# Optimization experiments

Measured on AMD Instinct MI355X. Metric: run time of the kernel, lower is better.

Reference implementation:

```python
import jax, jax.numpy as jnp
import numpy as np

B, T, D = 2, 2048, 1024
N, H = 16, 64  # num_heads, head_dim


def setup_inputs() -> dict:
    key = jax.random.key(0)
    ks = jax.random.split(key, 8)
    glorot = lambda k, shape, fan_in, fan_out: jax.random.uniform(
        k, shape, jnp.float32, -1.0, 1.0) * np.sqrt(6.0 / (fan_in + fan_out))
    return {
        "q": jax.random.normal(ks[0], (B, T, D), jnp.float32),
        "v": jax.random.normal(ks[1], (B, T, D), jnp.float32),
        "k": jax.random.normal(ks[2], (B, T, D), jnp.float32),
        "w_query": glorot(ks[3], (D, N, H), D, N * H),
        "b_query": jnp.zeros((N, 1, H), jnp.float32),
        "w_value": glorot(ks[4], (D, N, H), D, N * H),
        "b_value": jnp.zeros((N, 1, H), jnp.float32),
        "w_key": glorot(ks[5], (D, N, H), D, N * H),
        "b_key": jnp.zeros((N, 1, H), jnp.float32),
        "w_projection": glorot(ks[6], (N, D, H), N * H, D),
        "b_projection": jnp.zeros((1, D), jnp.float32),
    }


def reference(q, v, k, w_query, b_query, w_value, b_value, w_key, b_key,
              w_projection, b_projection):
    # QKV projections: [B,T,D] x [D,N,H] -> [B,N,T,H]
    query = jnp.einsum('btd,dnh->bnth', q, w_query) + b_query
    value = jnp.einsum('btd,dnh->bnth', v, w_value) + b_value
    key_p = jnp.einsum('btd,dnh->bnth', k, w_key) + b_key
    # Scaled dot-product attention, scores divided by sqrt(head_dim)
    scale = 1.0 / jnp.sqrt(jnp.asarray(H, query.dtype))
    scores = jnp.einsum('bnth,bnsh->bnts', query, key_p) * scale  # [B,N,T,T]
    weights = jax.nn.softmax(scores, axis=-1)
    attn = jnp.einsum('bnts,bnsh->bnth', weights, value)
    # Output projection: [B,N,T,H] x [N,D,H] -> [B,T,D]
    out = jnp.einsum('bnth,ndh->btd', attn, w_projection) + b_projection
    return out
```

## Files before the change

### kernel.cpp

```cpp
#include <hip/hip_runtime.h>
#include <hip/hip_bf16.h>
#include <cstdint>
#include <cstddef>


typedef __attribute__((ext_vector_type(8))) short short8;
typedef __attribute__((ext_vector_type(4))) float floatx4;
typedef __attribute__((ext_vector_type(8))) unsigned short ushort8;

#define EXP2F(x) __builtin_amdgcn_exp2f(x)

static __device__ __forceinline__ unsigned short f2bf(float f) {
    union { float f; unsigned int u; } v; v.f = f;
    unsigned int r = v.u + 0x7fffu + ((v.u >> 16) & 1u);
    return (unsigned short)(r >> 16);
}
static __device__ __forceinline__ unsigned int pk2bf(float lo, float hi) {
    __hip_bfloat162 t = __float22bfloat162_rn(make_float2(lo, hi));
    union { __hip_bfloat162 h; unsigned int u; } c; c.h = t;
    return c.u;
}
static __device__ __forceinline__ void gl_lds16(const unsigned short* g, unsigned short* l) {
    __builtin_amdgcn_global_load_lds(
        (const __attribute__((address_space(1))) unsigned int*)g,
        (__attribute__((address_space(3))) unsigned int*)l, 16, 0, 0);
}

__global__ __launch_bounds__(256) void mha_transpose_w(
    const float* __restrict__ wq, const float* __restrict__ wk, const float* __restrict__ wv,
    unsigned short* __restrict__ wqT, unsigned short* __restrict__ wkT, unsigned short* __restrict__ wvT)
{
    __shared__ float tile[32][33];
    const float* src; unsigned short* dst;
    int z = blockIdx.z;
    if (z == 0)      { src = wq; dst = wqT; }
    else if (z == 1) { src = wk; dst = wkT; }
    else             { src = wv; dst = wvT; }
    int n0 = blockIdx.x * 32, d0 = blockIdx.y * 32;
    int tx = threadIdx.x, ty = threadIdx.y;
    #pragma unroll
    for (int j = 0; j < 4; ++j)
        tile[ty + j * 8][tx] = src[(size_t)(d0 + ty + j * 8) * 1024 + n0 + tx];
    __syncthreads();
    #pragma unroll
    for (int j = 0; j < 4; ++j)
        dst[(size_t)(n0 + ty + j * 8) * 1024 + d0 + tx] = f2bf(tile[tx][ty + j * 8]);
}

__global__ __launch_bounds__(256) void mha_reorder_wp(
    const float* __restrict__ wp, unsigned short* __restrict__ wp2)
{
    int base = blockIdx.x * 1024 + threadIdx.x;
    #pragma unroll
    for (int i = 0; i < 4; ++i) {
        int idx = base + i * 256;
        int n = idx >> 16, d = (idx >> 6) & 1023, h = idx & 63;
        wp2[(size_t)d * 1024 + n * 64 + h] = f2bf(wp[idx]);
    }
}

__global__ __launch_bounds__(256) void prep_bf16(
    const float* __restrict__ x, unsigned short* __restrict__ xb)
{
    size_t i = ((size_t)blockIdx.x * 256 + threadIdx.x) * 8;
    float4 a = *(const float4*)(x + i);
    float4 b = *(const float4*)(x + i + 4);
    uint4 o;
    o.x = pk2bf(a.x, a.y); o.y = pk2bf(a.z, a.w);
    o.z = pk2bf(b.x, b.y); o.w = pk2bf(b.z, b.w);
    *(uint4*)(xb + i) = o;
}

__global__ __launch_bounds__(256) void gemm_qkv64(
    const unsigned short* __restrict__ A0, const unsigned short* __restrict__ A1,
    const unsigned short* __restrict__ A2,
    const unsigned short* __restrict__ W0, const unsigned short* __restrict__ W1,
    const unsigned short* __restrict__ W2,
    const float* __restrict__ b0, const float* __restrict__ b1, const float* __restrict__ b2,
    unsigned short* __restrict__ O0, unsigned short* __restrict__ O1, unsigned short* __restrict__ O2,
    float qscale, int matSel)
{
    __shared__ unsigned short As[64 * 32];
    __shared__ unsigned short Bs[128 * 32];
    int bm = blockIdx.x, by = blockIdx.y;
    int mat, nt;
    if (matSel < 0) { mat = by >> 3; nt = by & 7; } else { mat = matSel; nt = by; }
    const unsigned short* A  = mat == 0 ? A0 : (mat == 1 ? A1 : A2);
    const unsigned short* WT = mat == 0 ? W0 : (mat == 1 ? W1 : W2);
    const float* bias        = mat == 0 ? b0 : (mat == 1 ? b1 : b2);
    unsigned short* Out      = mat == 0 ? O0 : (mat == 1 ? O1 : O2);
    float scale = (mat == 0) ? qscale : 1.0f;
    int vmode = (mat == 2);

    int tid = threadIdx.x;
    int w = tid >> 6, lane = tid & 63, c15 = lane & 15, quad = lane >> 4;
    int wm = w >> 1, wn = w & 1;

    const unsigned short* gsrc[3];
    unsigned short* ldst[3];
    #pragma unroll
    for (int j = 0; j < 3; ++j) {
        int c = w * 3 + j;
        if (c < 4) {
            gsrc[j] = A + (size_t)(bm * 64 + c * 16 + (lane >> 2)) * 1024 + (lane & 3) * 8;
            ldst[j] = &As[c * 512 + lane * 8];
        } else {
            int d = c - 4;
            gsrc[j] = WT + (size_t)(nt * 128 + d * 16 + (lane >> 2)) * 1024 + (lane & 3) * 8;
            ldst[j] = &Bs[d * 512 + lane * 8];
        }
    }

    floatx4 acc[2][4];
    #pragma unroll
    for (int mi = 0; mi < 2; ++mi)
        #pragma unroll
        for (int ni = 0; ni < 4; ++ni) acc[mi][ni] = (floatx4){0.f, 0.f, 0.f, 0.f};

    for (int kt = 0; kt < 32; ++kt) {
        __syncthreads();
        #pragma unroll
        for (int j = 0; j < 3; ++j) gl_lds16(gsrc[j] + kt * 32, ldst[j]);
        __syncthreads();
        short8 af[2], bfr[4];
        #pragma unroll
        for (int mi = 0; mi < 2; ++mi)
            af[mi] = *(const short8*)&As[(wm * 32 + mi * 16 + c15) * 32 + quad * 8];
        #pragma unroll
        for (int ni = 0; ni < 4; ++ni)
            bfr[ni] = *(const short8*)&Bs[(wn * 64 + ni * 16 + c15) * 32 + quad * 8];
        #pragma unroll
        for (int mi = 0; mi < 2; ++mi)
            #pragma unroll
            for (int ni = 0; ni < 4; ++ni)
                acc[mi][ni] = __builtin_amdgcn_mfma_f32_16x16x32_bf16(af[mi], bfr[ni], acc[mi][ni], 0, 0, 0);
    }
    #pragma unroll
    for (int mi = 0; mi < 2; ++mi)
        #pragma unroll
        for (int ni = 0; ni < 4; ++ni)
            #pragma unroll
            for (int r = 0; r < 4; ++r) {
                int row = bm * 64 + wm * 32 + mi * 16 + quad * 4 + r;
                int col = nt * 128 + wn * 64 + ni * 16 + c15;
                float val = (acc[mi][ni][r] + bias[col]) * scale;
                int b = row >> 11, t = row & 2047, n = col >> 6, h = col & 63;
                if (vmode)
                    Out[((size_t)(b * 16 + n) * 64 + h) * 2048 + t] = f2bf(val);
                else
                    Out[((size_t)(b * 16 + n) * 2048 + t) * 64 + h] = f2bf(val);
            }
}

__global__ __launch_bounds__(256) void mha_flash3(
    const unsigned short* __restrict__ Qp, const unsigned short* __restrict__ Kp,
    const unsigned short* __restrict__ Vt, unsigned short* __restrict__ attnb)
{
    __shared__ unsigned short Ks[64 * 72];
    __shared__ unsigned short Vs[64 * 72];
    __shared__ unsigned short Pl[4][32 * 72];

    int bi = blockIdx.x;
    int bn = bi >> 4, qt = bi & 15;
    int b = bn >> 4, n = bn & 15;
    int tid = threadIdx.x;
    int w = tid >> 6, lane = tid & 63, c15 = lane & 15, quad = lane >> 4;

    const unsigned short* Qb = Qp + (size_t)bn * 2048 * 64;
    const unsigned short* Kb = Kp + (size_t)bn * 2048 * 64;
    const unsigned short* Vb = Vt + (size_t)bn * 64 * 2048;

    int qbase = qt * 128 + w * 32;

    short8 bQ[2][2];
    #pragma unroll
    for (int tni = 0; tni < 2; ++tni)
        #pragma unroll
        for (int kc = 0; kc < 2; ++kc)
            bQ[tni][kc] = *(const short8*)(Qb + (size_t)(qbase + tni * 16 + c15) * 64 + kc * 32 + quad * 8);

    float l_i[2] = {0.f, 0.f};
    floatx4 o[2][4];
    #pragma unroll
    for (int i = 0; i < 2; ++i)
        #pragma unroll
        for (int j = 0; j < 4; ++j) o[i][j] = (floatx4){0.f, 0.f, 0.f, 0.f};

    unsigned short* Pw = &Pl[w][0];
    int srow = tid >> 3, scc = tid & 7;

    ushort8 kreg[2], vreg[2];
    #pragma unroll
    for (int i = 0; i < 2; ++i) {
        kreg[i] = *(const ushort8*)(Kb + (size_t)(srow + i * 32) * 64 + scc * 8);
        vreg[i] = *(const ushort8*)(Vb + (size_t)(srow + i * 32) * 2048 + scc * 8);
    }

    for (int it = 0; it < 32; ++it) {
        __syncthreads();
        #pragma unroll
        for (int i = 0; i < 2; ++i) {
            *(ushort8*)&Ks[(srow + i * 32) * 72 + scc * 8] = kreg[i];
            *(ushort8*)&Vs[(srow + i * 32) * 72 + scc * 8] = vreg[i];
        }
        if (it < 31) {
            int s1 = (it + 1) * 64;
            #pragma unroll
            for (int i = 0; i < 2; ++i) {
                kreg[i] = *(const ushort8*)(Kb + (size_t)(s1 + srow + i * 32) * 64 + scc * 8);
                vreg[i] = *(const ushort8*)(Vb + (size_t)(srow + i * 32) * 2048 + s1 + scc * 8);
            }
        }
        __syncthreads();

        floatx4 sc[4][2];
        #pragma unroll
        for (int smi = 0; smi < 4; ++smi) {
            short8 a0 = *(const short8*)&Ks[(smi * 16 + c15) * 72 + quad * 8];
            short8 a1 = *(const short8*)&Ks[(smi * 16 + c15) * 72 + 32 + quad * 8];
            #pragma unroll
            for (int tni = 0; tni < 2; ++tni) {
                floatx4 t = (floatx4){0.f, 0.f, 0.f, 0.f};
                t = __builtin_amdgcn_mfma_f32_16x16x32_bf16(a0, bQ[tni][0], t, 0, 0, 0);
                t = __builtin_amdgcn_mfma_f32_16x16x32_bf16(a1, bQ[tni][1], t, 0, 0, 0);
                sc[smi][tni] = t;
            }
        }
        #pragma unroll
        for (int tni = 0; tni < 2; ++tni) {
            float rs = 0.f;
            #pragma unroll
            for (int smi = 0; smi < 4; ++smi) {
                float p0 = EXP2F(sc[smi][tni][0]);
                float p1 = EXP2F(sc[smi][tni][1]);
                float p2 = EXP2F(sc[smi][tni][2]);
                float p3 = EXP2F(sc[smi][tni][3]);
                rs += (p0 + p1) + (p2 + p3);
                uint2 pw;
                pw.x = pk2bf(p0, p1);
                pw.y = pk2bf(p2, p3);
                *(uint2*)&Pw[(tni * 16 + c15) * 72 + smi * 16 + quad * 4] = pw;
            }
            l_i[tni] += rs;
        }
        short8 bv[4][2];
        #pragma unroll
        for (int hni = 0; hni < 4; ++hni)
            #pragma unroll
            for (int kc = 0; kc < 2; ++kc)
                bv[hni][kc] = *(const short8*)&Vs[(hni * 16 + c15) * 72 + kc * 32 + quad * 8];
        #pragma unroll
        for (int tmi = 0; tmi < 2; ++tmi) {
            short8 ap0 = *(const short8*)&Pw[(tmi * 16 + c15) * 72 + quad * 8];
            short8 ap1 = *(const short8*)&Pw[(tmi * 16 + c15) * 72 + 32 + quad * 8];
            #pragma unroll
            for (int hni = 0; hni < 4; ++hni) {
                o[tmi][hni] = __builtin_amdgcn_mfma_f32_16x16x32_bf16(ap0, bv[hni][0], o[tmi][hni], 0, 0, 0);
                o[tmi][hni] = __builtin_amdgcn_mfma_f32_16x16x32_bf16(ap1, bv[hni][1], o[tmi][hni], 0, 0, 0);
            }
        }
    }
    float lf[2];
    #pragma unroll
    for (int tmi = 0; tmi < 2; ++tmi) {
        float s = l_i[tmi];
        s += __shfl_xor(s, 16, 64);
        s += __shfl_xor(s, 32, 64);
        lf[tmi] = s;
    }
    #pragma unroll
    for (int tmi = 0; tmi < 2; ++tmi)
        #pragma unroll
        for (int r = 0; r < 4; ++r) {
            float linv = 1.0f / __shfl(lf[tmi], quad * 4 + r, 64);
            int t = qbase + tmi * 16 + quad * 4 + r;
            #pragma unroll
            for (int hni = 0; hni < 4; ++hni) {
                int col = n * 64 + hni * 16 + c15;
                attnb[(size_t)(b * 2048 + t) * 1024 + col] = f2bf(o[tmi][hni][r] * linv);
            }
        }
}

__global__ __launch_bounds__(256) void gemm_out64(
    const unsigned short* __restrict__ A, const unsigned short* __restrict__ BT,
    const float* __restrict__ bias, float* __restrict__ out)
{
    __shared__ unsigned short As[64 * 32];
    __shared__ unsigned short Bs[128 * 32];
    int bm = blockIdx.x, nt = blockIdx.y;
    int tid = threadIdx.x;
    int w = tid >> 6, lane = tid & 63, c15 = lane & 15, quad = lane >> 4;
    int wm = w >> 1, wn = w & 1;

    const unsigned short* gsrc[3];
    unsigned short* ldst[3];
    #pragma unroll
    for (int j = 0; j < 3; ++j) {
        int c = w * 3 + j;
        if (c < 4) {
            gsrc[j] = A + (size_t)(bm * 64 + c * 16 + (lane >> 2)) * 1024 + (lane & 3) * 8;
            ldst[j] = &As[c * 512 + lane * 8];
        } else {
            int d = c - 4;
            gsrc[j] = BT + (size_t)(nt * 128 + d * 16 + (lane >> 2)) * 1024 + (lane & 3) * 8;
            ldst[j] = &Bs[d * 512 + lane * 8];
        }
    }

    floatx4 acc[2][4];
    #pragma unroll
    for (int mi = 0; mi < 2; ++mi)
        #pragma unroll
        for (int ni = 0; ni < 4; ++ni) acc[mi][ni] = (floatx4){0.f, 0.f, 0.f, 0.f};

    for (int kt = 0; kt < 32; ++kt) {
        __syncthreads();
        #pragma unroll
        for (int j = 0; j < 3; ++j) gl_lds16(gsrc[j] + kt * 32, ldst[j]);
        __syncthreads();
        short8 af[2], bfr[4];
        #pragma unroll
        for (int mi = 0; mi < 2; ++mi)
            af[mi] = *(const short8*)&As[(wm * 32 + mi * 16 + c15) * 32 + quad * 8];
        #pragma unroll
        for (int ni = 0; ni < 4; ++ni)
            bfr[ni] = *(const short8*)&Bs[(wn * 64 + ni * 16 + c15) * 32 + quad * 8];
        #pragma unroll
        for (int mi = 0; mi < 2; ++mi)
            #pragma unroll
            for (int ni = 0; ni < 4; ++ni)
                acc[mi][ni] = __builtin_amdgcn_mfma_f32_16x16x32_bf16(af[mi], bfr[ni], acc[mi][ni], 0, 0, 0);
    }
    #pragma unroll
    for (int mi = 0; mi < 2; ++mi)
        #pragma unroll
        for (int ni = 0; ni < 4; ++ni)
            #pragma unroll
            for (int r = 0; r < 4; ++r) {
                int row = bm * 64 + wm * 32 + mi * 16 + quad * 4 + r;
                int col = nt * 128 + wn * 64 + ni * 16 + c15;
                out[(size_t)row * 1024 + col] = acc[mi][ni][r] + bias[col];
            }
}

extern "C" void kernel_launch(void* const* d_in, const int* in_sizes, int n_in,
                              void* d_out, int out_size, void* d_ws, size_t ws_size,
                              hipStream_t stream)
{
    const float* q  = (const float*)d_in[0];
    const float* v  = (const float*)d_in[1];
    const float* k  = (const float*)d_in[2];
    const float* wq = (const float*)d_in[3];
    const float* bq = (const float*)d_in[4];
    const float* wv = (const float*)d_in[5];
    const float* bv = (const float*)d_in[6];
    const float* wk = (const float*)d_in[7];
    const float* bk = (const float*)d_in[8];
    const float* wp = (const float*)d_in[9];
    const float* bp = (const float*)d_in[10];
    float* out = (float*)d_out;

    char* ws = (char*)d_ws;
    unsigned short* wqT  = (unsigned short*)(ws + (size_t)0);
    unsigned short* wkT  = (unsigned short*)(ws + ((size_t)2  << 20));
    unsigned short* wvT  = (unsigned short*)(ws + ((size_t)4  << 20));
    unsigned short* wp2  = (unsigned short*)(ws + ((size_t)6  << 20));
    unsigned short* Qp   = (unsigned short*)(ws + ((size_t)8  << 20));
    unsigned short* Kp   = (unsigned short*)(ws + ((size_t)16 << 20));
    unsigned short* Vtp  = (unsigned short*)(ws + ((size_t)24 << 20));
    unsigned short* Xb   = (unsigned short*)(ws + ((size_t)32 << 20));
    unsigned short* attnb= (unsigned short*)(ws + ((size_t)32 << 20));

    const float qscale = 0.125f * 1.44269504088896f;

    hipLaunchKernelGGL(mha_transpose_w, dim3(32, 32, 3), dim3(32, 8), 0, stream,
                       wq, wk, wv, wqT, wkT, wvT);
    hipLaunchKernelGGL(mha_reorder_wp, dim3(1024), dim3(256), 0, stream, wp, wp2);

    if (ws_size >= ((size_t)64 << 20)) {
        unsigned short* qb = (unsigned short*)(ws + ((size_t)40 << 20));
        unsigned short* kb = (unsigned short*)(ws + ((size_t)48 << 20));
        unsigned short* vb = (unsigned short*)(ws + ((size_t)56 << 20));
        hipLaunchKernelGGL(prep_bf16, dim3(2048), dim3(256), 0, stream, q, qb);
        hipLaunchKernelGGL(prep_bf16, dim3(2048), dim3(256), 0, stream, k, kb);
        hipLaunchKernelGGL(prep_bf16, dim3(2048), dim3(256), 0, stream, v, vb);
        hipLaunchKernelGGL(gemm_qkv64, dim3(64, 24), dim3(256), 0, stream,
                           qb, kb, vb, wqT, wkT, wvT, bq, bk, bv, Qp, Kp, Vtp, qscale, -1);
    } else {
        hipLaunchKernelGGL(prep_bf16, dim3(2048), dim3(256), 0, stream, q, Xb);
        hipLaunchKernelGGL(gemm_qkv64, dim3(64, 8), dim3(256), 0, stream,
                           Xb, Xb, Xb, wqT, wkT, wvT, bq, bk, bv, Qp, Kp, Vtp, qscale, 0);
        hipLaunchKernelGGL(prep_bf16, dim3(2048), dim3(256), 0, stream, k, Xb);
        hipLaunchKernelGGL(gemm_qkv64, dim3(64, 8), dim3(256), 0, stream,
                           Xb, Xb, Xb, wqT, wkT, wvT, bq, bk, bv, Qp, Kp, Vtp, qscale, 1);
        hipLaunchKernelGGL(prep_bf16, dim3(2048), dim3(256), 0, stream, v, Xb);
        hipLaunchKernelGGL(gemm_qkv64, dim3(64, 8), dim3(256), 0, stream,
                           Xb, Xb, Xb, wqT, wkT, wvT, bq, bk, bv, Qp, Kp, Vtp, qscale, 2);
    }

    hipLaunchKernelGGL(mha_flash3, dim3(512), dim3(256), 0, stream, Qp, Kp, Vtp, attnb);
    hipLaunchKernelGGL(gemm_out64, dim3(64, 8), dim3(256), 0, stream, attnb, wp2, bp, out);
}
```

Measured before the change: 251.7 us.

## Enlarge QKV GEMM tile, swizzle out-GEMM LDS, fuse prep launches, remap flash blocks to XCDs

The three bf16 conversion launches are merged into one 2D-grid kernel. The QKV GEMM moves to a 128x128 tile (4x4 MFMA per wave) for more data reuse per block, and the output GEMM takes a K-step of 64 with an XOR-swizzled LDS layout to reduce bank conflicts. The flash attention block index is remapped so that blocks sharing a head land on the same XCD, which should improve L2 locality. Larger tiles raise register and LDS pressure and halve the QKV grid, which may hurt occupancy.

```diff
diff --git a/kernel.cpp b/kernel.cpp
--- a/kernel.cpp
+++ b/kernel.cpp
@@ -59,19 +59,23 @@
     }
 }
 
-__global__ __launch_bounds__(256) void prep_bf16(
-    const float* __restrict__ x, unsigned short* __restrict__ xb)
-{
+__global__ __launch_bounds__(256) void prep_bf16_3(
+    const float* __restrict__ x0, const float* __restrict__ x1, const float* __restrict__ x2,
+    unsigned short* __restrict__ o0, unsigned short* __restrict__ o1, unsigned short* __restrict__ o2)
+{
+    int y = blockIdx.y;
+    const float* x = y == 0 ? x0 : (y == 1 ? x1 : x2);
+    unsigned short* o = y == 0 ? o0 : (y == 1 ? o1 : o2);
     size_t i = ((size_t)blockIdx.x * 256 + threadIdx.x) * 8;
     float4 a = *(const float4*)(x + i);
     float4 b = *(const float4*)(x + i + 4);
-    uint4 o;
-    o.x = pk2bf(a.x, a.y); o.y = pk2bf(a.z, a.w);
-    o.z = pk2bf(b.x, b.y); o.w = pk2bf(b.z, b.w);
-    *(uint4*)(xb + i) = o;
-}
-
-__global__ __launch_bounds__(256) void gemm_qkv64(
+    uint4 pk;
+    pk.x = pk2bf(a.x, a.y); pk.y = pk2bf(a.z, a.w);
+    pk.z = pk2bf(b.x, b.y); pk.w = pk2bf(b.z, b.w);
+    *(uint4*)(o + i) = pk;
+}
+
+__global__ __launch_bounds__(256) void gemm_qkv128(
     const unsigned short* __restrict__ A0, const unsigned short* __restrict__ A1,
     const unsigned short* __restrict__ A2,
     const unsigned short* __restrict__ W0, const unsigned short* __restrict__ W1,
@@ -80,7 +84,7 @@
     unsigned short* __restrict__ O0, unsigned short* __restrict__ O1, unsigned short* __restrict__ O2,
     float qscale, int matSel)
 {
-    __shared__ unsigned short As[64 * 32];
+    __shared__ unsigned short As[128 * 32];
     __shared__ unsigned short Bs[128 * 32];
     int bm = blockIdx.x, by = blockIdx.y;
     int mat, nt;
@@ -96,52 +100,48 @@
     int w = tid >> 6, lane = tid & 63, c15 = lane & 15, quad = lane >> 4;
     int wm = w >> 1, wn = w & 1;
 
-    const unsigned short* gsrc[3];
-    unsigned short* ldst[3];
-    #pragma unroll
-    for (int j = 0; j < 3; ++j) {
-        int c = w * 3 + j;
-        if (c < 4) {
-            gsrc[j] = A + (size_t)(bm * 64 + c * 16 + (lane >> 2)) * 1024 + (lane & 3) * 8;
-            ldst[j] = &As[c * 512 + lane * 8];
-        } else {
-            int d = c - 4;
-            gsrc[j] = WT + (size_t)(nt * 128 + d * 16 + (lane >> 2)) * 1024 + (lane & 3) * 8;
-            ldst[j] = &Bs[d * 512 + lane * 8];
-        }
-    }
-
-    floatx4 acc[2][4];
-    #pragma unroll
-    for (int mi = 0; mi < 2; ++mi)
+    const unsigned short* gA[2]; unsigned short* lA[2];
+    const unsigned short* gB[2]; unsigned short* lB[2];
+    #pragma unroll
+    for (int i = 0; i < 2; ++i) {
+        int s = (w * 2 + i) * 64 + lane;
+        gA[i] = A  + (size_t)(bm * 128 + (s >> 2)) * 1024 + (s & 3) * 8;
+        lA[i] = &As[s * 8];
+        gB[i] = WT + (size_t)(nt * 128 + (s >> 2)) * 1024 + (s & 3) * 8;
+        lB[i] = &Bs[s * 8];
+    }
+
+    floatx4 acc[4][4];
+    #pragma unroll
+    for (int mi = 0; mi < 4; ++mi)
         #pragma unroll
         for (int ni = 0; ni < 4; ++ni) acc[mi][ni] = (floatx4){0.f, 0.f, 0.f, 0.f};
 
     for (int kt = 0; kt < 32; ++kt) {
         __syncthreads();
         #pragma unroll
-        for (int j = 0; j < 3; ++j) gl_lds16(gsrc[j] + kt * 32, ldst[j]);
-        __syncthreads();
-        short8 af[2], bfr[4];
-        #pragma unroll
-        for (int mi = 0; mi < 2; ++mi)
-            af[mi] = *(const short8*)&As[(wm * 32 + mi * 16 + c15) * 32 + quad * 8];
+        for (int i = 0; i < 2; ++i) { gl_lds16(gA[i] + kt * 32, lA[i]); gl_lds16(gB[i] + kt * 32, lB[i]); }
+        __syncthreads();
+        short8 af[4], bfr[4];
+        #pragma unroll
+        for (int mi = 0; mi < 4; ++mi)
+            af[mi] = *(const short8*)&As[(wm * 64 + mi * 16 + c15) * 32 + quad * 8];
         #pragma unroll
         for (int ni = 0; ni < 4; ++ni)
             bfr[ni] = *(const short8*)&Bs[(wn * 64 + ni * 16 + c15) * 32 + quad * 8];
         #pragma unroll
-        for (int mi = 0; mi < 2; ++mi)
+        for (int mi = 0; mi < 4; ++mi)
             #pragma unroll
             for (int ni = 0; ni < 4; ++ni)
                 acc[mi][ni] = __builtin_amdgcn_mfma_f32_16x16x32_bf16(af[mi], bfr[ni], acc[mi][ni], 0, 0, 0);
     }
     #pragma unroll
-    for (int mi = 0; mi < 2; ++mi)
+    for (int mi = 0; mi < 4; ++mi)
         #pragma unroll
         for (int ni = 0; ni < 4; ++ni)
             #pragma unroll
             for (int r = 0; r < 4; ++r) {
-                int row = bm * 64 + wm * 32 + mi * 16 + quad * 4 + r;
+                int row = bm * 128 + wm * 64 + mi * 16 + quad * 4 + r;
                 int col = nt * 128 + wn * 64 + ni * 16 + c15;
                 float val = (acc[mi][ni][r] + bias[col]) * scale;
                 int b = row >> 11, t = row & 2047, n = col >> 6, h = col & 63;
@@ -161,7 +161,8 @@
     __shared__ unsigned short Pl[4][32 * 72];
 
     int bi = blockIdx.x;
-    int bn = bi >> 4, qt = bi & 15;
+    int xcd = bi & 7, j = bi >> 3;
+    int bn = xcd * 4 + (j >> 4), qt = j & 15;
     int b = bn >> 4, n = bn & 15;
     int tid = threadIdx.x;
     int w = tid >> 6, lane = tid & 63, c15 = lane & 15, quad = lane >> 4;
@@ -184,7 +185,7 @@
     #pragma unroll
     for (int i = 0; i < 2; ++i)
         #pragma unroll
-        for (int j = 0; j < 4; ++j) o[i][j] = (floatx4){0.f, 0.f, 0.f, 0.f};
+        for (int j2 = 0; j2 < 4; ++j2) o[i][j2] = (floatx4){0.f, 0.f, 0.f, 0.f};
 
     unsigned short* Pw = &Pl[w][0];
     int srow = tid >> 3, scc = tid & 7;
@@ -282,30 +283,32 @@
         }
 }
 
-__global__ __launch_bounds__(256) void gemm_out64(
+__global__ __launch_bounds__(256) void gemm_out64v2(
     const unsigned short* __restrict__ A, const unsigned short* __restrict__ BT,
     const float* __restrict__ bias, float* __restrict__ out)
 {
-    __shared__ unsigned short As[64 * 32];
-    __shared__ unsigned short Bs[128 * 32];
+    __shared__ unsigned short As[64 * 64];
+    __shared__ unsigned short Bs[128 * 64];
     int bm = blockIdx.x, nt = blockIdx.y;
     int tid = threadIdx.x;
     int w = tid >> 6, lane = tid & 63, c15 = lane & 15, quad = lane >> 4;
     int wm = w >> 1, wn = w & 1;
 
-    const unsigned short* gsrc[3];
-    unsigned short* ldst[3];
-    #pragma unroll
-    for (int j = 0; j < 3; ++j) {
-        int c = w * 3 + j;
-        if (c < 4) {
-            gsrc[j] = A + (size_t)(bm * 64 + c * 16 + (lane >> 2)) * 1024 + (lane & 3) * 8;
-            ldst[j] = &As[c * 512 + lane * 8];
-        } else {
-            int d = c - 4;
-            gsrc[j] = BT + (size_t)(nt * 128 + d * 16 + (lane >> 2)) * 1024 + (lane & 3) * 8;
-            ldst[j] = &Bs[d * 512 + lane * 8];
-        }
+    const unsigned short* gA[2]; unsigned short* lA[2];
+    const unsigned short* gB[4]; unsigned short* lB[4];
+    #pragma unroll
+    for (int i = 0; i < 2; ++i) {
+        int s = (w * 2 + i) * 64 + lane;
+        int row = s >> 3, cl = (s & 7) ^ (row & 7);
+        gA[i] = A + (size_t)(bm * 64 + row) * 1024 + cl * 8;
+        lA[i] = &As[s * 8];
+    }
+    #pragma unroll
+    for (int i = 0; i < 4; ++i) {
+        int s = (w * 4 + i) * 64 + lane;
+        int row = s >> 3, cl = (s & 7) ^ (row & 7);
+        gB[i] = BT + (size_t)(nt * 128 + row) * 1024 + cl * 8;
+        lB[i] = &Bs[s * 8];
     }
 
     floatx4 acc[2][4];
@@ -314,23 +317,32 @@
         #pragma unroll
         for (int ni = 0; ni < 4; ++ni) acc[mi][ni] = (floatx4){0.f, 0.f, 0.f, 0.f};
 
-    for (int kt = 0; kt < 32; ++kt) {
-        __syncthreads();
-        #pragma unroll
-        for (int j = 0; j < 3; ++j) gl_lds16(gsrc[j] + kt * 32, ldst[j]);
-        __syncthreads();
-        short8 af[2], bfr[4];
-        #pragma unroll
-        for (int mi = 0; mi < 2; ++mi)
-            af[mi] = *(const short8*)&As[(wm * 32 + mi * 16 + c15) * 32 + quad * 8];
-        #pragma unroll
-        for (int ni = 0; ni < 4; ++ni)
-            bfr[ni] = *(const short8*)&Bs[(wn * 64 + ni * 16 + c15) * 32 + quad * 8];
-        #pragma unroll
-        for (int mi = 0; mi < 2; ++mi)
-            #pragma unroll
-            for (int ni = 0; ni < 4; ++ni)
-                acc[mi][ni] = __builtin_amdgcn_mfma_f32_16x16x32_bf16(af[mi], bfr[ni], acc[mi][ni], 0, 0, 0);
+    for (int kt = 0; kt < 16; ++kt) {
+        __syncthreads();
+        #pragma unroll
+        for (int i = 0; i < 2; ++i) gl_lds16(gA[i] + kt * 64, lA[i]);
+        #pragma unroll
+        for (int i = 0; i < 4; ++i) gl_lds16(gB[i] + kt * 64, lB[i]);
+        __syncthreads();
+        #pragma unroll
+        for (int kc = 0; kc < 2; ++kc) {
+            short8 af[2], bfr[4];
+            #pragma unroll
+            for (int mi = 0; mi < 2; ++mi) {
+                int row = wm * 32 + mi * 16 + c15;
+                af[mi] = *(const short8*)&As[row * 64 + (((kc * 4 + quad) ^ (row & 7)) * 8)];
+            }
+            #pragma unroll
+            for (int ni = 0; ni < 4; ++ni) {
+                int row = wn * 64 + ni * 16 + c15;
+                bfr[ni] = *(const short8*)&Bs[row * 64 + (((kc * 4 + quad) ^ (row & 7)) * 8)];
+            }
+            #pragma unroll
+            for (int mi = 0; mi < 2; ++mi)
+                #pragma unroll
+                for (int ni = 0; ni < 4; ++ni)
+                    acc[mi][ni] = __builtin_amdgcn_mfma_f32_16x16x32_bf16(af[mi], bfr[ni], acc[mi][ni], 0, 0, 0);
+        }
     }
     #pragma unroll
     for (int mi = 0; mi < 2; ++mi)
@@ -382,23 +394,21 @@
         unsigned short* qb = (unsigned short*)(ws + ((size_t)40 << 20));
         unsigned short* kb = (unsigned short*)(ws + ((size_t)48 << 20));
         unsigned short* vb = (unsigned short*)(ws + ((size_t)56 << 20));
-        hipLaunchKernelGGL(prep_bf16, dim3(2048), dim3(256), 0, stream, q, qb);
-        hipLaunchKernelGGL(prep_bf16, dim3(2048), dim3(256), 0, stream, k, kb);
-        hipLaunchKernelGGL(prep_bf16, dim3(2048), dim3(256), 0, stream, v, vb);
-        hipLaunchKernelGGL(gemm_qkv64, dim3(64, 24), dim3(256), 0, stream,
+        hipLaunchKernelGGL(prep_bf16_3, dim3(2048, 3), dim3(256), 0, stream, q, k, v, qb, kb, vb);
+        hipLaunchKernelGGL(gemm_qkv128, dim3(32, 24), dim3(256), 0, stream,
                            qb, kb, vb, wqT, wkT, wvT, bq, bk, bv, Qp, Kp, Vtp, qscale, -1);
     } else {
-        hipLaunchKernelGGL(prep_bf16, dim3(2048), dim3(256), 0, stream, q, Xb);
-        hipLaunchKernelGGL(gemm_qkv64, dim3(64, 8), dim3(256), 0, stream,
+        hipLaunchKernelGGL(prep_bf16_3, dim3(2048, 1), dim3(256), 0, stream, q, q, q, Xb, Xb, Xb);
+        hipLaunchKernelGGL(gemm_qkv128, dim3(32, 8), dim3(256), 0, stream,
                            Xb, Xb, Xb, wqT, wkT, wvT, bq, bk, bv, Qp, Kp, Vtp, qscale, 0);
-        hipLaunchKernelGGL(prep_bf16, dim3(2048), dim3(256), 0, stream, k, Xb);
-        hipLaunchKernelGGL(gemm_qkv64, dim3(64, 8), dim3(256), 0, stream,
+        hipLaunchKernelGGL(prep_bf16_3, dim3(2048, 1), dim3(256), 0, stream, k, k, k, Xb, Xb, Xb);
+        hipLaunchKernelGGL(gemm_qkv128, dim3(32, 8), dim3(256), 0, stream,
                            Xb, Xb, Xb, wqT, wkT, wvT, bq, bk, bv, Qp, Kp, Vtp, qscale, 1);
-        hipLaunchKernelGGL(prep_bf16, dim3(2048), dim3(256), 0, stream, v, Xb);
-        hipLaunchKernelGGL(gemm_qkv64, dim3(64, 8), dim3(256), 0, stream,
+        hipLaunchKernelGGL(prep_bf16_3, dim3(2048, 1), dim3(256), 0, stream, v, v, v, Xb, Xb, Xb);
+        hipLaunchKernelGGL(gemm_qkv128, dim3(32, 8), dim3(256), 0, stream,
                            Xb, Xb, Xb, wqT, wkT, wvT, bq, bk, bv, Qp, Kp, Vtp, qscale, 2);
     }
 
     hipLaunchKernelGGL(mha_flash3, dim3(512), dim3(256), 0, stream, Qp, Kp, Vtp, attnb);
-    hipLaunchKernelGGL(gemm_out64, dim3(64, 8), dim3(256), 0, stream, attnb, wp2, bp, out);
-}
+    hipLaunchKernelGGL(gemm_out64v2, dim3(64, 8), dim3(256), 0, stream, attnb, wp2, bp, out);
+}
```

Result: faster. 226.4 us (-10.1%).
